# Optimization experiments

Hardware: AMD Instinct MI355X
Metric: run time of the kernel (lower is better)

## Reference

```python
import jax, jax.numpy as jnp
import numpy as np

N_NODES = 100000
MEM_DIM = 256
MSG_DIM = 256
HID_DIM = 256
DIVIDE = 8
B = 20000


def setup_inputs() -> dict:
    key = jax.random.key(0)
    ks = jax.random.split(key, 10)
    memory = jax.random.normal(ks[0], (N_NODES, MEM_DIM), jnp.float32)
    # unique node ids per step (module assumes uniqueness within a batch)
    node_ids = jax.vmap(lambda k: jax.random.permutation(k, N_NODES)[:B])(
        jax.random.split(ks[1], DIVIDE)).astype(jnp.int64)
    messages = jax.random.normal(ks[2], (DIVIDE, B, MSG_DIM), jnp.float32)
    dtdg_output = jax.random.normal(ks[3], (N_NODES, HID_DIM), jnp.float32)
    s_c = 1.0 / np.sqrt(MSG_DIM)
    s_d = 1.0 / np.sqrt(HID_DIM)
    s_h = 1.0 / np.sqrt(MEM_DIM)
    W_C_w = jax.random.uniform(ks[4], (2 * MEM_DIM, MSG_DIM), jnp.float32, -s_c, s_c)
    W_C_b = jax.random.uniform(ks[5], (2 * MEM_DIM,), jnp.float32, -s_c, s_c)
    W_D_w = jax.random.uniform(ks[6], (2 * MEM_DIM, HID_DIM), jnp.float32, -s_d, s_d)
    W_D_b = jax.random.uniform(ks[7], (2 * MEM_DIM,), jnp.float32, -s_d, s_d)
    W_h_w = jax.random.uniform(ks[8], (4 * MEM_DIM, MEM_DIM), jnp.float32, -s_h, s_h)
    W_h_b = jax.random.uniform(ks[9], (4 * MEM_DIM,), jnp.float32, -s_h, s_h)
    return dict(memory=memory, node_ids=node_ids, messages=messages,
                dtdg_output=dtdg_output, W_C_w=W_C_w, W_C_b=W_C_b,
                W_D_w=W_D_w, W_D_b=W_D_b, W_h_w=W_h_w, W_h_b=W_h_b)


def reference(memory, node_ids, messages, dtdg_output,
              W_C_w, W_C_b, W_D_w, W_D_b, W_h_w, W_h_b):
    M = memory.shape[1]

    def step(mem, xs):
        ids, msg = xs
        i_C = msg @ W_C_w.T + W_C_b                 # [B, 2M]
        m_g = mem[ids]                               # gather [B, M]
        h = m_g @ W_h_w.T + W_h_b                    # [B, 4M]
        gate_C = jax.nn.sigmoid(i_C[:, :M] + h[:, M:2 * M])
        h_C = jnp.tanh(i_C[:, M:] + h[:, 3 * M:])
        new = (1.0 - gate_C) * h_C + gate_C * m_g
        return mem.at[ids].set(new), None

    # first divide-1 sequential CTDT updates
    mem, _ = jax.lax.scan(step, memory, (node_ids[:-1], messages[:-1]))

    # final step fuses CTDT message and DTDG output
    ids = node_ids[-1]
    msg = messages[-1]
    i_C = msg @ W_C_w.T + W_C_b                      # [B, 2M]
    i_D = dtdg_output[ids] @ W_D_w.T + W_D_b         # [B, 2M]
    m_g = mem[ids]                                   # [B, M]
    h = m_g @ W_h_w.T + W_h_b                        # [B, 4M]
    Gate_D = jax.nn.sigmoid(i_D[:, :M] + h[:, :M])
    Gate_C = jax.nn.sigmoid(i_C[:, :M] + h[:, M:2 * M])
    h_D = jnp.tanh(i_D[:, M:] + h[:, 2 * M:3 * M])
    h_C = jnp.tanh(i_C[:, M:2 * M] + h[:, 3 * M:])
    out = Gate_D / 2 * h_D + Gate_C / 2 * h_C + (2.0 - Gate_D - Gate_C) / 2 * m_g
    return mem.at[ids].set(out)
```

## Files before the change

kernel.cpp:

```cpp
#include <hip/hip_runtime.h>
#include <math.h>

#define N_NODES 100000
#define B 20000
#define DIVIDE 8

typedef __attribute__((ext_vector_type(8))) short bf16x8;
typedef __attribute__((ext_vector_type(4))) float f32x4;

#define BPS_BYTES (16 * 32 * 64 * 16)
#define BPF_BYTES (24 * 64 * 64 * 16)
#define BIAS_S_BYTE (BPS_BYTES + BPF_BYTES)
#define BIAS_F_BYTE (BIAS_S_BYTE + 512 * 4)

__device__ __forceinline__ float fsigmoid(float x) {
    x = fminf(fmaxf(x, -30.f), 30.f);
    return 1.f / (1.f + __expf(-x));
}
__device__ __forceinline__ float ftanh(float x) {
    x = fminf(fmaxf(x, -15.f), 15.f);
    float e = __expf(2.f * x);
    return (e - 1.f) / (e + 1.f);
}
__device__ __forceinline__ short f2bf(float v) {
    unsigned u = __builtin_bit_cast(unsigned, v);
    u += 0x7FFFu + ((u >> 16) & 1u);
    return (short)(u >> 16);
}
__device__ __forceinline__ bf16x8 cvt8(float4 a, float4 b) {
    bf16x8 r;
    r[0] = f2bf(a.x); r[1] = f2bf(a.y); r[2] = f2bf(a.z); r[3] = f2bf(a.w);
    r[4] = f2bf(b.x); r[5] = f2bf(b.y); r[6] = f2bf(b.z); r[7] = f2bf(b.w);
    return r;
}


__global__ void prep_bps(const float* __restrict__ Wc, const float* __restrict__ Wcb,
                         const float* __restrict__ Wh, const float* __restrict__ Whb,
                         short* __restrict__ bps, float* __restrict__ bias) {
    int idx = blockIdx.x * 256 + threadIdx.x;
    int ks = idx >> 11;
    int ct = (idx >> 6) & 31;
    int lane = idx & 63;
    int k0 = ks * 32 + ((lane >> 4) << 3);
    int c = ct * 16 + (lane & 15);
    int j = c & 255;
    bool isH = c >= 256;
    bf16x8 o;
#pragma unroll
    for (int t = 0; t < 8; t++) {
        int k = k0 + t;
        float v;
        if (k < 256) v = Wc[(size_t)(isH ? 256 + j : j) * 256 + k];
        else         v = Wh[(size_t)(isH ? 768 + j : 256 + j) * 256 + (k - 256)];
        o[t] = f2bf(v);
    }
    *(bf16x8*)(bps + (size_t)idx * 8) = o;
    if (idx < 512) {
        float b = (idx < 256) ? (Wcb[idx] + Whb[256 + idx])
                              : (Wcb[256 + (idx - 256)] + Whb[768 + (idx - 256)]);
        bias[idx] = b;
    }
}

__global__ void prep_bpf(const float* __restrict__ Wc, const float* __restrict__ Wcb,
                         const float* __restrict__ Wd, const float* __restrict__ Wdb,
                         const float* __restrict__ Wh, const float* __restrict__ Whb,
                         short* __restrict__ bpf, float* __restrict__ bias) {
    int idx = blockIdx.x * 256 + threadIdx.x;
    int ks = idx >> 12;
    int ct = (idx >> 6) & 63;
    int lane = idx & 63;
    int k0 = ks * 32 + ((lane >> 4) << 3);
    int c = ct * 16 + (lane & 15);
    int sel = c >> 8, j = c & 255;
    bf16x8 o;
#pragma unroll
    for (int t = 0; t < 8; t++) {
        int k = k0 + t;
        float v = 0.f;
        if (k < 256) {
            if (sel == 0) v = Wc[(size_t)j * 256 + k];
            else if (sel == 1) v = Wc[(size_t)(256 + j) * 256 + k];
        } else if (k < 512) {
            int kk = k - 256;
            int row = (sel == 0) ? (256 + j) : (sel == 1) ? (768 + j)
                    : (sel == 2) ? j : (512 + j);
            v = Wh[(size_t)row * 256 + kk];
        } else {
            int kk = k - 512;
            if (sel == 2) v = Wd[(size_t)j * 256 + kk];
            else if (sel == 3) v = Wd[(size_t)(256 + j) * 256 + kk];
        }
        o[t] = f2bf(v);
    }
    *(bf16x8*)(bpf + (size_t)idx * 8) = o;
    if (idx < 1024) {
        int jj = idx & 255, s = idx >> 8;
        float b = (s == 0) ? (Wcb[jj] + Whb[256 + jj])
                : (s == 1) ? (Wcb[256 + jj] + Whb[768 + jj])
                : (s == 2) ? (Wdb[jj] + Whb[jj])
                           : (Wdb[256 + jj] + Whb[512 + jj]);
        bias[idx] = b;
    }
}

__global__ __launch_bounds__(512, 4) void step_mfma(
        float* __restrict__ mem, const float* __restrict__ msg,
        const int* __restrict__ ids,
        const bf16x8* __restrict__ Bp, const float* __restrict__ bias) {
    __shared__ int sIds[32];
    __shared__ short As[32 * 512];
    int tid = threadIdx.x;
    int r0 = blockIdx.x * 32;
    if (tid < 32) sIds[tid] = ids[r0 + tid];
    __syncthreads();

    float4 v0[4], v1[4];
    int gb[4];
#pragma unroll
    for (int j = 0; j < 4; j++) {
        int u = j * 512 + tid;
        int row = u >> 6;
        int k0 = (u & 63) * 8;
        const float* src = (k0 < 256)
            ? msg + (size_t)(r0 + row) * 256 + k0
            : mem + (size_t)sIds[row] * 256 + (k0 - 256);
        v0[j] = *(const float4*)src;
        v1[j] = *(const float4*)(src + 4);
        gb[j] = (row * 1024 + k0 * 2) ^ ((row & 7) << 4);
    }
#pragma unroll
    for (int j = 0; j < 4; j++)
        *(bf16x8*)((char*)As + gb[j]) = cvt8(v0[j], v1[j]);
    __syncthreads();

    int lane = tid & 63, q = tid >> 6;
    int cl = lane & 15, quad = lane >> 4;

    f32x4 accG[2][2] = {{{0.f}}};
    f32x4 accH[2][2] = {{{0.f}}};
    const bf16x8* bp = Bp + lane;

#pragma unroll
    for (int ks = 0; ks < 16; ks++) {
        bf16x8 a[2];
#pragma unroll
        for (int rt = 0; rt < 2; rt++) {
            int row = rt * 16 + cl;
            int ab = (row * 1024 + ks * 64 + quad * 16) ^ ((row & 7) << 4);
            a[rt] = *(const bf16x8*)((const char*)As + ab);
        }
        int base = ks * 32 * 64;
#pragma unroll
        for (int t = 0; t < 2; t++) {
            bf16x8 bg = bp[base + (q * 2 + t) * 64];
            bf16x8 bh = bp[base + (16 + q * 2 + t) * 64];
#pragma unroll
            for (int rt = 0; rt < 2; rt++) {
                accG[rt][t] = __builtin_amdgcn_mfma_f32_16x16x32_bf16(a[rt], bg, accG[rt][t], 0, 0, 0);
                accH[rt][t] = __builtin_amdgcn_mfma_f32_16x16x32_bf16(a[rt], bh, accH[rt][t], 0, 0, 0);
            }
        }
    }

#pragma unroll
    for (int t = 0; t < 2; t++) {
        int col = q * 32 + t * 16 + cl;
        float bg = bias[col], bh = bias[256 + col];
#pragma unroll
        for (int rt = 0; rt < 2; rt++) {
#pragma unroll
            for (int r = 0; r < 4; r++) {
                int id = sIds[rt * 16 + quad * 4 + r];
                float* p = mem + (size_t)id * 256 + col;
                float m = *p;
                float g = fsigmoid(accG[rt][t][r] + bg);
                float h = ftanh(accH[rt][t][r] + bh);
                *p = (1.f - g) * h + g * m;
            }
        }
    }
}

__global__ __launch_bounds__(512, 4) void final_mfma(
        float* __restrict__ mem, const float* __restrict__ msg,
        const int* __restrict__ ids, const float* __restrict__ dtdg,
        const bf16x8* __restrict__ Bp, const float* __restrict__ bias) {
    __shared__ int sIds[32];
    __shared__ short As[32 * 768];
    int tid = threadIdx.x;
    int r0 = blockIdx.x * 32;
    if (tid < 32) sIds[tid] = ids[r0 + tid];
    __syncthreads();

    float4 v0[6], v1[6];
    int gb[6];
#pragma unroll
    for (int j = 0; j < 6; j++) {
        int u = j * 512 + tid;
        int row = u / 96;
        int k0 = (u % 96) * 8;
        const float* src;
        if (k0 < 256)      src = msg + (size_t)(r0 + row) * 256 + k0;
        else if (k0 < 512) src = mem + (size_t)sIds[row] * 256 + (k0 - 256);
        else               src = dtdg + (size_t)sIds[row] * 256 + (k0 - 512);
        v0[j] = *(const float4*)src;
        v1[j] = *(const float4*)(src + 4);
        gb[j] = (row * 1536 + k0 * 2) ^ ((row & 7) << 4);
    }
#pragma unroll
    for (int j = 0; j < 6; j++)
        *(bf16x8*)((char*)As + gb[j]) = cvt8(v0[j], v1[j]);
    __syncthreads();

    int lane = tid & 63, q = tid >> 6;
    int cl = lane & 15, quad = lane >> 4;

    f32x4 aGC[2][2] = {{{0.f}}}, aHC[2][2] = {{{0.f}}};
    f32x4 aGD[2][2] = {{{0.f}}}, aHD[2][2] = {{{0.f}}};
    const bf16x8* bp = Bp + lane;

#pragma unroll
    for (int ks = 0; ks < 24; ks++) {
        bf16x8 a[2];
#pragma unroll
        for (int rt = 0; rt < 2; rt++) {
            int row = rt * 16 + cl;
            int ab = (row * 1536 + ks * 64 + quad * 16) ^ ((row & 7) << 4);
            a[rt] = *(const bf16x8*)((const char*)As + ab);
        }
        int base = ks * 64 * 64;
#pragma unroll
        for (int t = 0; t < 2; t++) {
            int ctb = 2 * q + t;
            if (ks < 16) {
                bf16x8 b0 = bp[base + ctb * 64];
                bf16x8 b1 = bp[base + (16 + ctb) * 64];
#pragma unroll
                for (int rt = 0; rt < 2; rt++) {
                    aGC[rt][t] = __builtin_amdgcn_mfma_f32_16x16x32_bf16(a[rt], b0, aGC[rt][t], 0, 0, 0);
                    aHC[rt][t] = __builtin_amdgcn_mfma_f32_16x16x32_bf16(a[rt], b1, aHC[rt][t], 0, 0, 0);
                }
            }
            if (ks >= 8) {
                bf16x8 b2 = bp[base + (32 + ctb) * 64];
                bf16x8 b3 = bp[base + (48 + ctb) * 64];
#pragma unroll
                for (int rt = 0; rt < 2; rt++) {
                    aGD[rt][t] = __builtin_amdgcn_mfma_f32_16x16x32_bf16(a[rt], b2, aGD[rt][t], 0, 0, 0);
                    aHD[rt][t] = __builtin_amdgcn_mfma_f32_16x16x32_bf16(a[rt], b3, aHD[rt][t], 0, 0, 0);
                }
            }
        }
    }

#pragma unroll
    for (int t = 0; t < 2; t++) {
        int col = q * 32 + t * 16 + cl;
        float b0 = bias[col], b1 = bias[256 + col];
        float b2 = bias[512 + col], b3 = bias[768 + col];
#pragma unroll
        for (int rt = 0; rt < 2; rt++) {
#pragma unroll
            for (int r = 0; r < 4; r++) {
                int id = sIds[rt * 16 + quad * 4 + r];
                float* p = mem + (size_t)id * 256 + col;
                float m = *p;
                float gc = fsigmoid(aGC[rt][t][r] + b0);
                float hc = ftanh(aHC[rt][t][r] + b1);
                float gd = fsigmoid(aGD[rt][t][r] + b2);
                float hd = ftanh(aHD[rt][t][r] + b3);
                *p = m + 0.5f * (gc * (hc - m) + gd * (hd - m));
            }
        }
    }
}

extern "C" void kernel_launch(void* const* d_in, const int* in_sizes, int n_in,
                              void* d_out, int out_size, void* d_ws, size_t ws_size,
                              hipStream_t stream) {
    (void)in_sizes; (void)n_in; (void)out_size; (void)ws_size;
    const float* memory = (const float*)d_in[0];
    const int* node_ids = (const int*)d_in[1];
    const float* messages = (const float*)d_in[2];
    const float* dtdg = (const float*)d_in[3];
    const float* Wc = (const float*)d_in[4];
    const float* Wcb = (const float*)d_in[5];
    const float* Wd = (const float*)d_in[6];
    const float* Wdb = (const float*)d_in[7];
    const float* Wh = (const float*)d_in[8];
    const float* Whb = (const float*)d_in[9];
    float* mem = (float*)d_out;
    char* ws = (char*)d_ws;

    short* bps = (short*)ws;
    short* bpf = (short*)(ws + BPS_BYTES);
    float* bias_s = (float*)(ws + BIAS_S_BYTE);
    float* bias_f = (float*)(ws + BIAS_F_BYTE);

    hipMemcpyAsync(mem, memory, (size_t)N_NODES * 256 * sizeof(float),
                   hipMemcpyDeviceToDevice, stream);

    prep_bps<<<128, 256, 0, stream>>>(Wc, Wcb, Wh, Whb, bps, bias_s);
    prep_bpf<<<384, 256, 0, stream>>>(Wc, Wcb, Wd, Wdb, Wh, Whb, bpf, bias_f);

    for (int t = 0; t < DIVIDE - 1; t++) {
        step_mfma<<<B / 32, 512, 0, stream>>>(
            mem, messages + (size_t)t * B * 256, node_ids + (size_t)t * B,
            (const bf16x8*)bps, bias_s);
    }
    final_mfma<<<B / 32, 512, 0, stream>>>(
        mem, messages + (size_t)(DIVIDE - 1) * B * 256,
        node_ids + (size_t)(DIVIDE - 1) * B, dtdg,
        (const bf16x8*)bpf, bias_f);
}
```

Before: 632.1 us.

## Fuse initial memory copy into first step and overlap gathers with MFMA

After: 629.1 us. Within noise of the previous version (-0.5%).

```diff
diff --git a/kernel.cpp b/kernel.cpp
--- a/kernel.cpp
+++ b/kernel.cpp
@@ -4,6 +4,8 @@
 #define N_NODES 100000
 #define B 20000
 #define DIVIDE 8
+#define NTILES (B / 32)
+#define NCOPYBLK ((N_NODES + 63) / 64)
 
 typedef __attribute__((ext_vector_type(8))) short bf16x8;
 typedef __attribute__((ext_vector_type(4))) float f32x4;
@@ -12,6 +14,7 @@
 #define BPF_BYTES (24 * 64 * 64 * 16)
 #define BIAS_S_BYTE (BPS_BYTES + BPF_BYTES)
 #define BIAS_F_BYTE (BIAS_S_BYTE + 512 * 4)
+#define FLAGS_BYTE  (BIAS_F_BYTE + 4096)
 
 __device__ __forceinline__ float fsigmoid(float x) {
     x = fminf(fmaxf(x, -30.f), 30.f);
@@ -33,7 +36,6 @@
     r[4] = f2bf(b.x); r[5] = f2bf(b.y); r[6] = f2bf(b.z); r[7] = f2bf(b.w);
     return r;
 }
-
 
 __global__ void prep_bps(const float* __restrict__ Wc, const float* __restrict__ Wcb,
                          const float* __restrict__ Wh, const float* __restrict__ Whb,
@@ -105,34 +107,55 @@
     }
 }
 
-__global__ __launch_bounds__(512, 4) void step_mfma(
-        float* __restrict__ mem, const float* __restrict__ msg,
-        const int* __restrict__ ids,
-        const bf16x8* __restrict__ Bp, const float* __restrict__ bias) {
+__global__ void set_flags(const int* __restrict__ ids, unsigned char* __restrict__ flags) {
+    int i = blockIdx.x * 256 + threadIdx.x;
+    if (i < B) flags[ids[i]] = 1;
+}
+
+__global__ __launch_bounds__(512, 4) void step_fused(
+        const float* __restrict__ gsrc, float* __restrict__ mem,
+        const float* __restrict__ msg, const int* __restrict__ ids,
+        const bf16x8* __restrict__ Bp, const float* __restrict__ bias,
+        const float* __restrict__ msrc, const unsigned char* __restrict__ flags) {
+    int tid = threadIdx.x;
+    if (blockIdx.x >= NTILES) {
+        int row = (blockIdx.x - NTILES) * 64 + (tid >> 3);
+        if (row < N_NODES && !flags[row]) {
+            const float4* s = (const float4*)(msrc + (size_t)row * 256);
+            float4* d = (float4*)(mem + (size_t)row * 256);
+            int c0 = tid & 7;
+#pragma unroll
+            for (int j = 0; j < 8; j++) d[c0 + j * 8] = s[c0 + j * 8];
+        }
+        return;
+    }
     __shared__ int sIds[32];
     __shared__ short As[32 * 512];
-    int tid = threadIdx.x;
     int r0 = blockIdx.x * 32;
     if (tid < 32) sIds[tid] = ids[r0 + tid];
     __syncthreads();
 
-    float4 v0[4], v1[4];
-    int gb[4];
-#pragma unroll
-    for (int j = 0; j < 4; j++) {
-        int u = j * 512 + tid;
-        int row = u >> 6;
-        int k0 = (u & 63) * 8;
-        const float* src = (k0 < 256)
-            ? msg + (size_t)(r0 + row) * 256 + k0
-            : mem + (size_t)sIds[row] * 256 + (k0 - 256);
-        v0[j] = *(const float4*)src;
-        v1[j] = *(const float4*)(src + 4);
-        gb[j] = (row * 1024 + k0 * 2) ^ ((row & 7) << 4);
-    }
-#pragma unroll
-    for (int j = 0; j < 4; j++)
-        *(bf16x8*)((char*)As + gb[j]) = cvt8(v0[j], v1[j]);
+    float4 a0[2], a1[2]; int ab_[2];
+#pragma unroll
+    for (int j = 0; j < 2; j++) {
+        int i = j * 512 + tid;
+        int row = i >> 5, k0 = (i & 31) * 8;
+        const float* s = msg + (size_t)(r0 + row) * 256 + k0;
+        a0[j] = *(const float4*)s; a1[j] = *(const float4*)(s + 4);
+        ab_[j] = (row * 1024 + k0 * 2) ^ ((row & 7) << 4);
+    }
+    float4 g0[2], g1[2]; int gb_[2];
+#pragma unroll
+    for (int j = 0; j < 2; j++) {
+        int i = j * 512 + tid;
+        int row = i >> 5, k = (i & 31) * 8;
+        const float* s = gsrc + (size_t)sIds[row] * 256 + k;
+        g0[j] = *(const float4*)s; g1[j] = *(const float4*)(s + 4);
+        gb_[j] = (row * 1024 + 512 + k * 2) ^ ((row & 7) << 4);
+    }
+#pragma unroll
+    for (int j = 0; j < 2; j++)
+        *(bf16x8*)((char*)As + ab_[j]) = cvt8(a0[j], a1[j]);
     __syncthreads();
 
     int lane = tid & 63, q = tid >> 6;
@@ -143,7 +166,7 @@
     const bf16x8* bp = Bp + lane;
 
 #pragma unroll
-    for (int ks = 0; ks < 16; ks++) {
+    for (int ks = 0; ks < 8; ks++) {
         bf16x8 a[2];
 #pragma unroll
         for (int rt = 0; rt < 2; rt++) {
@@ -163,6 +186,41 @@
             }
         }
     }
+#pragma unroll
+    for (int j = 0; j < 2; j++)
+        *(bf16x8*)((char*)As + gb_[j]) = cvt8(g0[j], g1[j]);
+    float mpre[2][2][4];
+#pragma unroll
+    for (int t = 0; t < 2; t++)
+#pragma unroll
+        for (int rt = 0; rt < 2; rt++)
+#pragma unroll
+            for (int r = 0; r < 4; r++)
+                mpre[t][rt][r] = gsrc[(size_t)sIds[rt * 16 + quad * 4 + r] * 256
+                                      + q * 32 + t * 16 + cl];
+    __syncthreads();
+
+#pragma unroll
+    for (int ks = 8; ks < 16; ks++) {
+        bf16x8 a[2];
+#pragma unroll
+        for (int rt = 0; rt < 2; rt++) {
+            int row = rt * 16 + cl;
+            int ab = (row * 1024 + ks * 64 + quad * 16) ^ ((row & 7) << 4);
+            a[rt] = *(const bf16x8*)((const char*)As + ab);
+        }
+        int base = ks * 32 * 64;
+#pragma unroll
+        for (int t = 0; t < 2; t++) {
+            bf16x8 bg = bp[base + (q * 2 + t) * 64];
+            bf16x8 bh = bp[base + (16 + q * 2 + t) * 64];
+#pragma unroll
+            for (int rt = 0; rt < 2; rt++) {
+                accG[rt][t] = __builtin_amdgcn_mfma_f32_16x16x32_bf16(a[rt], bg, accG[rt][t], 0, 0, 0);
+                accH[rt][t] = __builtin_amdgcn_mfma_f32_16x16x32_bf16(a[rt], bh, accH[rt][t], 0, 0, 0);
+            }
+        }
+    }
 
 #pragma unroll
     for (int t = 0; t < 2; t++) {
@@ -173,11 +231,10 @@
 #pragma unroll
             for (int r = 0; r < 4; r++) {
                 int id = sIds[rt * 16 + quad * 4 + r];
-                float* p = mem + (size_t)id * 256 + col;
-                float m = *p;
+                float m = mpre[t][rt][r];
                 float g = fsigmoid(accG[rt][t][r] + bg);
                 float h = ftanh(accH[rt][t][r] + bh);
-                *p = (1.f - g) * h + g * m;
+                mem[(size_t)id * 256 + col] = (1.f - g) * h + g * m;
             }
         }
     }
@@ -194,24 +251,27 @@
     if (tid < 32) sIds[tid] = ids[r0 + tid];
     __syncthreads();
 
-    float4 v0[6], v1[6];
-    int gb[6];
-#pragma unroll
-    for (int j = 0; j < 6; j++) {
-        int u = j * 512 + tid;
-        int row = u / 96;
-        int k0 = (u % 96) * 8;
-        const float* src;
-        if (k0 < 256)      src = msg + (size_t)(r0 + row) * 256 + k0;
-        else if (k0 < 512) src = mem + (size_t)sIds[row] * 256 + (k0 - 256);
-        else               src = dtdg + (size_t)sIds[row] * 256 + (k0 - 512);
-        v0[j] = *(const float4*)src;
-        v1[j] = *(const float4*)(src + 4);
-        gb[j] = (row * 1536 + k0 * 2) ^ ((row & 7) << 4);
-    }
-#pragma unroll
-    for (int j = 0; j < 6; j++)
-        *(bf16x8*)((char*)As + gb[j]) = cvt8(v0[j], v1[j]);
+    float4 a0[2], a1[2]; int ab_[2];
+#pragma unroll
+    for (int j = 0; j < 2; j++) {
+        int i = j * 512 + tid;
+        int row = i >> 5, k0 = (i & 31) * 8;
+        const float* s = msg + (size_t)(r0 + row) * 256 + k0;
+        a0[j] = *(const float4*)s; a1[j] = *(const float4*)(s + 4);
+        ab_[j] = (row * 1536 + k0 * 2) ^ ((row & 7) << 4);
+    }
+    float4 g0[2], g1[2]; int gb_[2];
+#pragma unroll
+    for (int j = 0; j < 2; j++) {
+        int i = j * 512 + tid;
+        int row = i >> 5, k = (i & 31) * 8;
+        const float* s = mem + (size_t)sIds[row] * 256 + k;
+        g0[j] = *(const float4*)s; g1[j] = *(const float4*)(s + 4);
+        gb_[j] = (row * 1536 + 512 + k * 2) ^ ((row & 7) << 4);
+    }
+#pragma unroll
+    for (int j = 0; j < 2; j++)
+        *(bf16x8*)((char*)As + ab_[j]) = cvt8(a0[j], a1[j]);
     __syncthreads();
 
     int lane = tid & 63, q = tid >> 6;
@@ -222,7 +282,7 @@
     const bf16x8* bp = Bp + lane;
 
 #pragma unroll
-    for (int ks = 0; ks < 24; ks++) {
+    for (int ks = 0; ks < 8; ks++) {
         bf16x8 a[2];
 #pragma unroll
         for (int rt = 0; rt < 2; rt++) {
@@ -234,23 +294,89 @@
 #pragma unroll
         for (int t = 0; t < 2; t++) {
             int ctb = 2 * q + t;
-            if (ks < 16) {
-                bf16x8 b0 = bp[base + ctb * 64];
-                bf16x8 b1 = bp[base + (16 + ctb) * 64];
-#pragma unroll
-                for (int rt = 0; rt < 2; rt++) {
-                    aGC[rt][t] = __builtin_amdgcn_mfma_f32_16x16x32_bf16(a[rt], b0, aGC[rt][t], 0, 0, 0);
-                    aHC[rt][t] = __builtin_amdgcn_mfma_f32_16x16x32_bf16(a[rt], b1, aHC[rt][t], 0, 0, 0);
-                }
-            }
-            if (ks >= 8) {
-                bf16x8 b2 = bp[base + (32 + ctb) * 64];
-                bf16x8 b3 = bp[base + (48 + ctb) * 64];
-#pragma unroll
-                for (int rt = 0; rt < 2; rt++) {
-                    aGD[rt][t] = __builtin_amdgcn_mfma_f32_16x16x32_bf16(a[rt], b2, aGD[rt][t], 0, 0, 0);
-                    aHD[rt][t] = __builtin_amdgcn_mfma_f32_16x16x32_bf16(a[rt], b3, aHD[rt][t], 0, 0, 0);
-                }
+            bf16x8 b0 = bp[base + ctb * 64];
+            bf16x8 b1 = bp[base + (16 + ctb) * 64];
+#pragma unroll
+            for (int rt = 0; rt < 2; rt++) {
+                aGC[rt][t] = __builtin_amdgcn_mfma_f32_16x16x32_bf16(a[rt], b0, aGC[rt][t], 0, 0, 0);
+                aHC[rt][t] = __builtin_amdgcn_mfma_f32_16x16x32_bf16(a[rt], b1, aHC[rt][t], 0, 0, 0);
+            }
+        }
+    }
+#pragma unroll
+    for (int j = 0; j < 2; j++)
+        *(bf16x8*)((char*)As + gb_[j]) = cvt8(g0[j], g1[j]);
+    float mpre[2][2][4];
+#pragma unroll
+    for (int t = 0; t < 2; t++)
+#pragma unroll
+        for (int rt = 0; rt < 2; rt++)
+#pragma unroll
+            for (int r = 0; r < 4; r++)
+                mpre[t][rt][r] = mem[(size_t)sIds[rt * 16 + quad * 4 + r] * 256
+                                     + q * 32 + t * 16 + cl];
+    __syncthreads();
+
+#pragma unroll
+    for (int ks = 8; ks < 16; ks++) {
+        bf16x8 a[2];
+#pragma unroll
+        for (int rt = 0; rt < 2; rt++) {
+            int row = rt * 16 + cl;
+            int ab = (row * 1536 + ks * 64 + quad * 16) ^ ((row & 7) << 4);
+            a[rt] = *(const bf16x8*)((const char*)As + ab);
+        }
+        int base = ks * 64 * 64;
+#pragma unroll
+        for (int t = 0; t < 2; t++) {
+            int ctb = 2 * q + t;
+            bf16x8 b0 = bp[base + ctb * 64];
+            bf16x8 b1 = bp[base + (16 + ctb) * 64];
+            bf16x8 b2 = bp[base + (32 + ctb) * 64];
+            bf16x8 b3 = bp[base + (48 + ctb) * 64];
+#pragma unroll
+            for (int rt = 0; rt < 2; rt++) {
+                aGC[rt][t] = __builtin_amdgcn_mfma_f32_16x16x32_bf16(a[rt], b0, aGC[rt][t], 0, 0, 0);
+                aHC[rt][t] = __builtin_amdgcn_mfma_f32_16x16x32_bf16(a[rt], b1, aHC[rt][t], 0, 0, 0);
+                aGD[rt][t] = __builtin_amdgcn_mfma_f32_16x16x32_bf16(a[rt], b2, aGD[rt][t], 0, 0, 0);
+                aHD[rt][t] = __builtin_amdgcn_mfma_f32_16x16x32_bf16(a[rt], b3, aHD[rt][t], 0, 0, 0);
+            }
+        }
+    }
+
+    float4 d0[2], d1[2]; int db_[2];
+#pragma unroll
+    for (int j = 0; j < 2; j++) {
+        int i = j * 512 + tid;
+        int row = i >> 5, k = (i & 31) * 8;
+        const float* s = dtdg + (size_t)sIds[row] * 256 + k;
+        d0[j] = *(const float4*)s; d1[j] = *(const float4*)(s + 4);
+        db_[j] = (row * 1536 + 1024 + k * 2) ^ ((row & 7) << 4);
+    }
+#pragma unroll
+    for (int j = 0; j < 2; j++)
+        *(bf16x8*)((char*)As + db_[j]) = cvt8(d0[j], d1[j]);
+    __syncthreads();
+
+#pragma unroll
+    for (int ks = 16; ks < 24; ks++) {
+        bf16x8 a[2];
+#pragma unroll
+        for (int rt = 0; rt < 2; rt++) {
+            int row = rt * 16 + cl;
+            int ab = (row * 1536 + ks * 64 + quad * 16) ^ ((row & 7) << 4);
+            a[rt] = *(const bf16x8*)((const char*)As + ab);
+        }
+        int base = ks * 64 * 64;
+#pragma unroll
+        for (int t = 0; t < 2; t++) {
+            int ctb = 2 * q + t;
+            bf16x8 b2 = bp[base + (32 + ctb) * 64];
+            bf16x8 b3 = bp[base + (48 + ctb) * 64];
+#pragma unroll
+            for (int rt = 0; rt < 2; rt++) {
+                aGD[rt][t] = __builtin_amdgcn_mfma_f32_16x16x32_bf16(a[rt], b2, aGD[rt][t], 0, 0, 0);
+                aHD[rt][t] = __builtin_amdgcn_mfma_f32_16x16x32_bf16(a[rt], b3, aHD[rt][t], 0, 0, 0);
             }
         }
     }
@@ -265,13 +391,12 @@
 #pragma unroll
             for (int r = 0; r < 4; r++) {
                 int id = sIds[rt * 16 + quad * 4 + r];
-                float* p = mem + (size_t)id * 256 + col;
-                float m = *p;
+                float m = mpre[t][rt][r];
                 float gc = fsigmoid(aGC[rt][t][r] + b0);
                 float hc = ftanh(aHC[rt][t][r] + b1);
                 float gd = fsigmoid(aGD[rt][t][r] + b2);
                 float hd = ftanh(aHD[rt][t][r] + b3);
-                *p = m + 0.5f * (gc * (hc - m) + gd * (hd - m));
+                mem[(size_t)id * 256 + col] = m + 0.5f * (gc * (hc - m) + gd * (hd - m));
             }
         }
     }
@@ -298,19 +423,24 @@
     short* bpf = (short*)(ws + BPS_BYTES);
     float* bias_s = (float*)(ws + BIAS_S_BYTE);
     float* bias_f = (float*)(ws + BIAS_F_BYTE);
-
-    hipMemcpyAsync(mem, memory, (size_t)N_NODES * 256 * sizeof(float),
-                   hipMemcpyDeviceToDevice, stream);
+    unsigned char* flags = (unsigned char*)(ws + FLAGS_BYTE);
+
+    hipMemsetAsync(flags, 0, N_NODES, stream);
+    set_flags<<<(B + 255) / 256, 256, 0, stream>>>(node_ids, flags);
 
     prep_bps<<<128, 256, 0, stream>>>(Wc, Wcb, Wh, Whb, bps, bias_s);
     prep_bpf<<<384, 256, 0, stream>>>(Wc, Wcb, Wd, Wdb, Wh, Whb, bpf, bias_f);
 
-    for (int t = 0; t < DIVIDE - 1; t++) {
-        step_mfma<<<B / 32, 512, 0, stream>>>(
-            mem, messages + (size_t)t * B * 256, node_ids + (size_t)t * B,
-            (const bf16x8*)bps, bias_s);
-    }
-    final_mfma<<<B / 32, 512, 0, stream>>>(
+    step_fused<<<NTILES + NCOPYBLK, 512, 0, stream>>>(
+        memory, mem, messages, node_ids,
+        (const bf16x8*)bps, bias_s, memory, flags);
+
+    for (int t = 1; t < DIVIDE - 1; t++) {
+        step_fused<<<NTILES, 512, 0, stream>>>(
+            mem, mem, messages + (size_t)t * B * 256, node_ids + (size_t)t * B,
+            (const bf16x8*)bps, bias_s, nullptr, nullptr);
+    }
+    final_mfma<<<NTILES, 512, 0, stream>>>(
         mem, messages + (size_t)(DIVIDE - 1) * B * 256,
         node_ids + (size_t)(DIVIDE - 1) * B, dtdg,
         (const bf16x8*)bpf, bias_f);
```
